# Optimization experiments

Hardware: AMD Instinct MI355X
Metric: run time of the kernel (lower is better)

The kernel has to match this reference:

```python
import jax, jax.numpy as jnp
import numpy as np

NUM_HEADS = 16

def setup_inputs() -> dict:
    key = jax.random.key(0)
    ks = jax.random.split(key, 5)
    B, N, C = 2, 2048, 1024
    x = jax.random.normal(ks[0], (B, N, C), dtype=jnp.float32)
    s_in = 1.0 / np.sqrt(C)
    Wq = jax.random.normal(ks[1], (C, 2 * C), dtype=jnp.float32) * s_in
    Wk = jax.random.normal(ks[2], (C, 2 * C), dtype=jnp.float32) * s_in
    Wv = jax.random.normal(ks[3], (C, 2 * C), dtype=jnp.float32) * s_in
    Wo = jax.random.normal(ks[4], (2 * C, C), dtype=jnp.float32) * (1.0 / np.sqrt(2 * C))
    return {"x": x, "Wq": Wq, "Wk": Wk, "Wv": Wv, "Wo": Wo}

def reference(x, Wq, Wk, Wv, Wo):
    B, N, C = x.shape
    H = NUM_HEADS
    hd = C // H  # head_dim
    def proj(W):
        # [B,N,2C] -> [B,H,N,2*hd]
        return (x @ W).reshape(B, N, H, 2 * hd).transpose(0, 2, 1, 3)
    q = proj(Wq)
    k = proj(Wk)
    v = proj(Wv)
    q_r, q_i = q[..., :hd], q[..., hd:]
    k_r, k_i = k[..., :hd], k[..., hd:]
    v_r, v_i = v[..., :hd], v[..., hd:]
    # complex inner product real part: Re(Q K^H) = q_r.k_r + q_i.k_i
    scores = (jnp.einsum('bhnd,bhmd->bhnm', q_r, k_r)
              + jnp.einsum('bhnd,bhmd->bhnm', q_i, k_i)) / jnp.sqrt(jnp.float32(hd))
    causal = jnp.tril(jnp.ones((N, N), dtype=bool))  # [N,N]
    scores = jnp.where(causal[None, None], scores, -jnp.inf)
    probs = jax.nn.softmax(scores, axis=-1)  # dropout off (eval mode)
    out_r = jnp.einsum('bhnm,bhmd->bhnd', probs, v_r)
    out_i = jnp.einsum('bhnm,bhmd->bhnd', probs, v_i)
    out = jnp.concatenate([out_r, out_i], axis=-1)  # [B,H,N,2*hd]
    out = out.transpose(0, 2, 1, 3).reshape(B, N, 2 * C)
    return out @ Wo  # [B,N,C]
```

## Files before the change

### kernel.cpp

```cpp
#include <hip/hip_runtime.h>
#include <hip/hip_bf16.h>
#include <stdint.h>
#include <cmath>

using bf16 = __hip_bfloat16;
typedef __attribute__((ext_vector_type(8))) short bf16x8;
typedef __attribute__((ext_vector_type(4))) short bf16x4;
typedef __attribute__((ext_vector_type(4))) float f32x4;

#define MFMA16(a, b, c) __builtin_amdgcn_mfma_f32_16x16x32_bf16(a, b, c, 0, 0, 0)

#if defined(__has_builtin)
#if __has_builtin(__builtin_amdgcn_mfma_f32_16x16x16bf16_1k)
#define HAVE_MFMA_K16 1
#endif
#endif
#ifndef HAVE_MFMA_K16
#define HAVE_MFMA_K16 0
#endif

#define NEG_BIG (-1e30f)

__device__ __forceinline__ short f2bf(float v) {
  return __builtin_bit_cast(short, __float2bfloat16(v));
}

__device__ __forceinline__ f32x4 pv_mfma(bf16x4 va, bf16x4 pb, f32x4 c) {
#if HAVE_MFMA_K16
  return __builtin_amdgcn_mfma_f32_16x16x16bf16_1k(va, pb, c, 0, 0, 0);
#else
  const bf16x8 a = {va[0], va[1], va[2], va[3], 0, 0, 0, 0};
  const bf16x8 b = {pb[0], pb[1], pb[2], pb[3], 0, 0, 0, 0};
  return MFMA16(a, b, c);
#endif
}

__device__ __forceinline__ void async_ld16(const bf16* g, bf16* l) {
  __builtin_amdgcn_global_load_lds(
      (const __attribute__((address_space(1))) unsigned int*)g,
      (__attribute__((address_space(3))) unsigned int*)l, 16, 0, 0);
}

template <typename T> __device__ __forceinline__ T cvt_out(float v);
template <> __device__ __forceinline__ float cvt_out<float>(float v) { return v; }
template <> __device__ __forceinline__ bf16 cvt_out<bf16>(float v) { return __float2bfloat16(v); }

__global__ void prep(const float* __restrict__ x,
                     const float* __restrict__ Wq, const float* __restrict__ Wk,
                     const float* __restrict__ Wv, const float* __restrict__ Wo,
                     bf16* __restrict__ xb, bf16* __restrict__ tq,
                     bf16* __restrict__ tk, bf16* __restrict__ tv,
                     bf16* __restrict__ to_) {
  __shared__ bf16 tile[32][33];
  const int bid = blockIdx.x;
  if (bid < 8192) {
    const int z = bid >> 11, tt = bid & 2047;
    const float* in = z == 0 ? Wq : z == 1 ? Wk : z == 2 ? Wv : Wo;
    bf16* out = z == 0 ? tq : z == 1 ? tk : z == 2 ? tv : to_;
    int R, Cc, c0, r0;
    if (z < 3) { R = 1024; Cc = 2048; c0 = (tt & 63) * 32; r0 = (tt >> 6) * 32; }
    else       { R = 2048; Cc = 1024; c0 = (tt & 31) * 32; r0 = (tt >> 5) * 32; }
    const int xx = threadIdx.x & 31;
    const int y = threadIdx.x >> 5;
#pragma unroll
    for (int yy = y; yy < 32; yy += 8)
      tile[yy][xx] = __float2bfloat16(in[(size_t)(r0 + yy) * Cc + c0 + xx]);
    __syncthreads();
#pragma unroll
    for (int yy = y; yy < 32; yy += 8)
      out[(size_t)(c0 + yy) * R + r0 + xx] = tile[xx][yy];
  } else {
    const int i = (bid - 8192) * 256 + threadIdx.x;
    const float4 v = ((const float4*)x)[i];
    bf16 o[4] = {__float2bfloat16(v.x), __float2bfloat16(v.y),
                 __float2bfloat16(v.z), __float2bfloat16(v.w)};
    *(uint64_t*)&xb[i * 4] = *(const uint64_t*)o;
  }
}

__global__ __launch_bounds__(256)
void gemm_qkv(const bf16* __restrict__ xb, const bf16* __restrict__ wq,
              const bf16* __restrict__ wk, const bf16* __restrict__ wv,
              bf16* __restrict__ qo, bf16* __restrict__ ko, bf16* __restrict__ vo) {
  __shared__ __align__(16) bf16 As[128 * 32];
  __shared__ __align__(16) bf16 Bs[128 * 32];
  const int op = blockIdx.y;
  const int bid = blockIdx.x;
  const bf16 *A, *B;
  int m0, n0;
  if (op < 2) { A = xb; B = op ? wk : wq; m0 = (bid >> 4) * 128; n0 = (bid & 15) * 128; }
  else        { A = wv; B = xb;           m0 = (bid & 15) * 128; n0 = (bid >> 4) * 128; }
  const int K = 1024;

  const int t = threadIdx.x;
  const int l = t & 63, w = t >> 6;
  const int q4 = l >> 4, li = l & 15;
  const int wr = (w >> 1) * 64, wc = (w & 1) * 64;

  f32x4 acc[4][4] = {};
  const int colst = (t & 3) * 8;
  const bf16* gA = A + (size_t)m0 * K;
  const bf16* gB = B + (size_t)n0 * K;

  for (int k0 = 0; k0 < K; k0 += 32) {
#pragma unroll
    for (int p = 0; p < 2; ++p) {
      const int row = p * 64 + (t >> 2);
      const int lbase = p * 2048 + (t & ~63) * 8;
      async_ld16(gA + (size_t)row * K + k0 + colst, &As[lbase]);
      async_ld16(gB + (size_t)row * K + k0 + colst, &Bs[lbase]);
    }
    __syncthreads();
    bf16x8 af[4], bfr[4];
#pragma unroll
    for (int i = 0; i < 4; ++i)
      af[i] = *(const bf16x8*)&As[(wr + i * 16 + li) * 32 + q4 * 8];
#pragma unroll
    for (int j = 0; j < 4; ++j)
      bfr[j] = *(const bf16x8*)&Bs[(wc + j * 16 + li) * 32 + q4 * 8];
#pragma unroll
    for (int i = 0; i < 4; ++i)
#pragma unroll
      for (int j = 0; j < 4; ++j)
        acc[i][j] = MFMA16(af[i], bfr[j], acc[i][j]);
    __syncthreads();
  }

#pragma unroll
  for (int i = 0; i < 4; ++i)
#pragma unroll
    for (int j = 0; j < 4; ++j)
#pragma unroll
      for (int r = 0; r < 4; ++r) {
        const int gm = m0 + wr + i * 16 + q4 * 4 + r;
        const int gn = n0 + wc + j * 16 + li;
        const bf16 v = __float2bfloat16(acc[i][j][r]);
        if (op < 2) {
          const int b = gm >> 11, nn = gm & 2047;
          const int h = gn >> 7, d = gn & 127;
          (op ? ko : qo)[((size_t)(b * 16 + h) * 2048 + nn) * 128 + d] = v;
        } else {
          const int h = gm >> 7, d = gm & 127;
          const int b = gn >> 11, nn = gn & 2047;
          vo[((size_t)(b * 16 + h) * 128 + d) * 2048 + nn] = v;
        }
      }
}

template <int NT, typename OT>
__global__ __launch_bounds__(256)
void gemm_bt(const bf16* __restrict__ A, const bf16* __restrict__ B,
             OT* __restrict__ C, int M, int N, int K) {
  __shared__ __align__(16) bf16 As[128 * 32];
  __shared__ __align__(16) bf16 Bs[NT * 32];
  constexpr int JN = NT / 32;
  const int t = threadIdx.x;
  const int l = t & 63, w = t >> 6;
  const int q4 = l >> 4, li = l & 15;
  const int m0 = blockIdx.y * 128;
  const int n0 = blockIdx.x * NT;
  const int wr = (w >> 1) * 64, wc = (w & 1) * (NT / 2);

  f32x4 acc[4][JN] = {};
  const int colst = (t & 3) * 8;
  const bf16* gA = A + (size_t)m0 * K;
  const bf16* gB = B + (size_t)n0 * K;

  for (int k0 = 0; k0 < K; k0 += 32) {
#pragma unroll
    for (int p = 0; p < 2; ++p) {
      const int row = p * 64 + (t >> 2);
      const int lbase = p * 2048 + (t & ~63) * 8;
      async_ld16(gA + (size_t)row * K + k0 + colst, &As[lbase]);
    }
#pragma unroll
    for (int p = 0; p < NT / 64; ++p) {
      const int row = p * 64 + (t >> 2);
      const int lbase = p * 2048 + (t & ~63) * 8;
      async_ld16(gB + (size_t)row * K + k0 + colst, &Bs[lbase]);
    }
    __syncthreads();
    bf16x8 af[4], bfr[JN];
#pragma unroll
    for (int i = 0; i < 4; ++i)
      af[i] = *(const bf16x8*)&As[(wr + i * 16 + li) * 32 + q4 * 8];
#pragma unroll
    for (int j = 0; j < JN; ++j)
      bfr[j] = *(const bf16x8*)&Bs[(wc + j * 16 + li) * 32 + q4 * 8];
#pragma unroll
    for (int i = 0; i < 4; ++i)
#pragma unroll
      for (int j = 0; j < JN; ++j)
        acc[i][j] = MFMA16(af[i], bfr[j], acc[i][j]);
    __syncthreads();
  }

#pragma unroll
  for (int i = 0; i < 4; ++i)
#pragma unroll
    for (int j = 0; j < JN; ++j)
#pragma unroll
      for (int r = 0; r < 4; ++r) {
        const int gm = m0 + wr + i * 16 + q4 * 4 + r;
        const int gn = n0 + wc + j * 16 + li;
        C[(size_t)gm * N + gn] = cvt_out<OT>(acc[i][j][r]);
      }
}

#define VSTR 72

__global__ __launch_bounds__(256, 2)
void flash_attn(const bf16* __restrict__ qm, const bf16* __restrict__ km,
                const bf16* __restrict__ vtm, bf16* __restrict__ om) {
  __shared__ __align__(16) bf16 Ks[64 * 128];
  __shared__ __align__(16) bf16 Vts[128 * VSTR];

  const int t = threadIdx.x;
  const int l = t & 63, w = t >> 6;
  const int q4 = l >> 4, li = l & 15;
  const int bh = blockIdx.x;
  const int y = blockIdx.y;
  const int qt = (y < 8) ? 15 - y : y - 8;
  const int qs = qt * 128;
  const size_t qkbase = (size_t)bh * 2048 * 128;
  const size_t vbase = (size_t)bh * 128 * 2048;
  const int b = bh >> 4, h = bh & 15;

  bf16x8 qf[2][4];
#pragma unroll
  for (int g = 0; g < 2; ++g) {
    const bf16* Qb = qm + qkbase + (size_t)(qs + w * 32 + g * 16 + li) * 128;
#pragma unroll
    for (int f = 0; f < 4; ++f)
      qf[g][f] = *(const bf16x8*)(Qb + f * 32 + q4 * 8);
  }

  f32x4 O[2][8] = {};
  float mrun[2] = {NEG_BIG, NEG_BIG}, lrun[2] = {0.f, 0.f};
  const int gmq[2] = {qs + w * 32 + li, qs + w * 32 + 16 + li};

  const int ktmax = 2 * qt + 1;
  for (int kt = 0; kt <= ktmax; ++kt) {
    const int kn = kt * 64;
#pragma unroll
    for (int p = 0; p < 4; ++p) {
      const int L = p * 256 + t;
      {
        const int row = L >> 4, c = L & 15;
        *(bf16x8*)&Ks[row * 128 + ((c ^ (row & 7)) * 8)] =
            *(const bf16x8*)(km + qkbase + (size_t)(kn + row) * 128 + c * 8);
      }
      {
        const int row = L >> 3, c = L & 7;
        *(bf16x8*)&Vts[row * VSTR + c * 8] =
            *(const bf16x8*)(vtm + vbase + (size_t)row * 2048 + kn + c * 8);
      }
    }
    __syncthreads();

    f32x4 S[2][4];
#pragma unroll
    for (int jk = 0; jk < 4; ++jk) {
      bf16x8 kf[4];
#pragma unroll
      for (int f = 0; f < 4; ++f)
        kf[f] = *(const bf16x8*)&Ks[(jk * 16 + li) * 128 + (((f * 4 + q4) ^ (li & 7)) * 8)];
#pragma unroll
      for (int g = 0; g < 2; ++g) {
        f32x4 s = {0.f, 0.f, 0.f, 0.f};
#pragma unroll
        for (int f = 0; f < 4; ++f) s = MFMA16(kf[f], qf[g][f], s);
        S[g][jk] = s;
      }
    }

    bf16x4 pb[2][4];
#pragma unroll
    for (int g = 0; g < 2; ++g) {
      const bool needmask = (kn + 63) > (qs + w * 32 + g * 16);
      float pv[16];
      float mx = NEG_BIG;
#pragma unroll
      for (int jk = 0; jk < 4; ++jk)
#pragma unroll
        for (int r = 0; r < 4; ++r) {
          float sv = S[g][jk][r] * 0.125f;
          if (needmask && (kn + jk * 16 + q4 * 4 + r) > gmq[g]) sv = NEG_BIG;
          pv[jk * 4 + r] = sv;
          mx = fmaxf(mx, sv);
        }
      mx = fmaxf(mx, __shfl_xor(mx, 16));
      mx = fmaxf(mx, __shfl_xor(mx, 32));
      const float nm = fmaxf(mrun[g], mx);
      const float alpha = __expf(mrun[g] - nm);
      mrun[g] = nm;
      float rs = 0.f;
#pragma unroll
      for (int jk = 0; jk < 4; ++jk)
#pragma unroll
        for (int r = 0; r < 4; ++r) {
          const float e = __expf(pv[jk * 4 + r] - nm);
          rs += e;
          pb[g][jk][r] = f2bf(e);
        }
      rs += __shfl_xor(rs, 16);
      rs += __shfl_xor(rs, 32);
      lrun[g] = lrun[g] * alpha + rs;
#pragma unroll
      for (int dt = 0; dt < 8; ++dt) O[g][dt] *= alpha;
    }

#pragma unroll
    for (int dt = 0; dt < 8; ++dt)
#pragma unroll
      for (int kc = 0; kc < 4; ++kc) {
        const bf16x4 va = *(const bf16x4*)&Vts[(dt * 16 + li) * VSTR + kc * 16 + q4 * 4];
        O[0][dt] = pv_mfma(va, pb[0][kc], O[0][dt]);
        O[1][dt] = pv_mfma(va, pb[1][kc], O[1][dt]);
      }
    __syncthreads();
  }

#pragma unroll
  for (int g = 0; g < 2; ++g) {
    const float inv = 1.0f / lrun[g];
    const size_t orow = (size_t)(b * 2048 + qs + w * 32 + g * 16 + li) * 2048 + h * 128;
#pragma unroll
    for (int dt = 0; dt < 8; ++dt) {
      bf16x4 o4;
#pragma unroll
      for (int r = 0; r < 4; ++r) o4[r] = f2bf(O[g][dt][r] * inv);
      *(bf16x4*)&om[orow + dt * 16 + q4 * 4] = o4;
    }
  }
}

extern "C" void kernel_launch(void* const* d_in, const int* in_sizes, int n_in,
                              void* d_out, int out_size, void* d_ws, size_t ws_size,
                              hipStream_t stream) {
  const float* x = (const float*)d_in[0];
  const float* Wq = (const float*)d_in[1];
  const float* Wk = (const float*)d_in[2];
  const float* Wv = (const float*)d_in[3];
  const float* Wo = (const float*)d_in[4];
  float* out = (float*)d_out;

  bf16* ws = (bf16*)d_ws;
  const size_t MEG = 1u << 20;
  bf16* xb = ws;
  bf16* wTq = ws + 4 * MEG;
  bf16* wTk = ws + 6 * MEG;
  bf16* wTv = ws + 8 * MEG;
  bf16* woT = ws + 10 * MEG;
  bf16* at_ws = ws + 2 * MEG;
  bf16* q_ws = ws + 12 * MEG;
  bf16* k_ws = ws + 20 * MEG;
  bf16* vt_ws = ws + 28 * MEG;

  const dim3 blk(256);

  prep<<<dim3(12288), blk, 0, stream>>>(x, Wq, Wk, Wv, Wo, xb, wTq, wTk, wTv, woT);
  gemm_qkv<<<dim3(512, 3), blk, 0, stream>>>(xb, wTq, wTk, wTv, q_ws, k_ws, vt_ws);
  flash_attn<<<dim3(32, 16), blk, 0, stream>>>(q_ws, k_ws, vt_ws, at_ws);
  gemm_bt<64, float><<<dim3(16, 32), blk, 0, stream>>>(at_ws, woT, out, 4096, 1024, 2048);
}
```

Measured before the change: 276.9 us.

## Use 128-wide KV tiles, exp2 softmax, lazy rescale, and swizzled V layout

Doubles the KV tile from 64 to 128 keys per iteration, which halves the loop trips and barriers. The V^T tile now uses an XOR-swizzled layout in place of the padded stride. Softmax folds the 1/sqrt(d) scale into a single exp2 FMA and masks only on the diagonal tile. The O/l rescale is skipped when no lane's running max moved. In exchange, LDS use grows to 64KB per block and register pressure rises, which may hurt occupancy with two blocks per CU.

```diff
diff --git a/kernel.cpp b/kernel.cpp
--- a/kernel.cpp
+++ b/kernel.cpp
@@ -14,12 +14,19 @@
 #if __has_builtin(__builtin_amdgcn_mfma_f32_16x16x16bf16_1k)
 #define HAVE_MFMA_K16 1
 #endif
+#if __has_builtin(__builtin_amdgcn_exp2f)
+#define EXP2F __builtin_amdgcn_exp2f
+#endif
 #endif
 #ifndef HAVE_MFMA_K16
 #define HAVE_MFMA_K16 0
 #endif
+#ifndef EXP2F
+#define EXP2F exp2f
+#endif
 
 #define NEG_BIG (-1e30f)
+#define K2SCALE 0.18033688011112042f
 
 __device__ __forceinline__ short f2bf(float v) {
   return __builtin_bit_cast(short, __float2bfloat16(v));
@@ -207,13 +214,11 @@
       }
 }
 
-#define VSTR 72
-
 __global__ __launch_bounds__(256, 2)
 void flash_attn(const bf16* __restrict__ qm, const bf16* __restrict__ km,
                 const bf16* __restrict__ vtm, bf16* __restrict__ om) {
-  __shared__ __align__(16) bf16 Ks[64 * 128];
-  __shared__ __align__(16) bf16 Vts[128 * VSTR];
+  __shared__ __align__(16) bf16 Ks[128 * 128];
+  __shared__ __align__(16) bf16 Vts[128 * 128];
 
   const int t = threadIdx.x;
   const int l = t & 63, w = t >> 6;
@@ -239,28 +244,23 @@
   float mrun[2] = {NEG_BIG, NEG_BIG}, lrun[2] = {0.f, 0.f};
   const int gmq[2] = {qs + w * 32 + li, qs + w * 32 + 16 + li};
 
-  const int ktmax = 2 * qt + 1;
-  for (int kt = 0; kt <= ktmax; ++kt) {
-    const int kn = kt * 64;
-#pragma unroll
-    for (int p = 0; p < 4; ++p) {
+  for (int kt = 0; kt <= qt; ++kt) {
+    const int kn = kt * 128;
+#pragma unroll
+    for (int p = 0; p < 8; ++p) {
       const int L = p * 256 + t;
-      {
-        const int row = L >> 4, c = L & 15;
-        *(bf16x8*)&Ks[row * 128 + ((c ^ (row & 7)) * 8)] =
-            *(const bf16x8*)(km + qkbase + (size_t)(kn + row) * 128 + c * 8);
-      }
-      {
-        const int row = L >> 3, c = L & 7;
-        *(bf16x8*)&Vts[row * VSTR + c * 8] =
-            *(const bf16x8*)(vtm + vbase + (size_t)row * 2048 + kn + c * 8);
-      }
-    }
-    __syncthreads();
-
-    f32x4 S[2][4];
-#pragma unroll
-    for (int jk = 0; jk < 4; ++jk) {
+      const int row = L >> 4, c = L & 15;
+      const int j = c ^ (row & 7);
+      *(bf16x8*)&Ks[row * 128 + j * 8] =
+          *(const bf16x8*)(km + qkbase + (size_t)(kn + row) * 128 + c * 8);
+      *(bf16x8*)&Vts[row * 128 + j * 8] =
+          *(const bf16x8*)(vtm + vbase + (size_t)row * 2048 + kn + c * 8);
+    }
+    __syncthreads();
+
+    f32x4 S[2][8];
+#pragma unroll
+    for (int jk = 0; jk < 8; ++jk) {
       bf16x8 kf[4];
 #pragma unroll
       for (int f = 0; f < 4; ++f)
@@ -274,47 +274,67 @@
       }
     }
 
-    bf16x4 pb[2][4];
+    const bool diag = (kt == qt);
+    bf16x4 pb[2][8];
+    float mold[2], nmv[2], rsv[2];
+    bool nomove = true;
 #pragma unroll
     for (int g = 0; g < 2; ++g) {
-      const bool needmask = (kn + 63) > (qs + w * 32 + g * 16);
-      float pv[16];
+      if (diag) {
+#pragma unroll
+        for (int jk = 0; jk < 8; ++jk)
+#pragma unroll
+          for (int r = 0; r < 4; ++r)
+            if ((kn + jk * 16 + q4 * 4 + r) > gmq[g]) S[g][jk][r] = NEG_BIG;
+      }
       float mx = NEG_BIG;
 #pragma unroll
-      for (int jk = 0; jk < 4; ++jk)
-#pragma unroll
-        for (int r = 0; r < 4; ++r) {
-          float sv = S[g][jk][r] * 0.125f;
-          if (needmask && (kn + jk * 16 + q4 * 4 + r) > gmq[g]) sv = NEG_BIG;
-          pv[jk * 4 + r] = sv;
-          mx = fmaxf(mx, sv);
-        }
+      for (int jk = 0; jk < 8; ++jk) {
+        mx = fmaxf(mx, fmaxf(fmaxf(S[g][jk][0], S[g][jk][1]),
+                             fmaxf(S[g][jk][2], S[g][jk][3])));
+      }
       mx = fmaxf(mx, __shfl_xor(mx, 16));
       mx = fmaxf(mx, __shfl_xor(mx, 32));
+      mold[g] = mrun[g];
       const float nm = fmaxf(mrun[g], mx);
-      const float alpha = __expf(mrun[g] - nm);
+      nomove = nomove && (mx <= mold[g]);
       mrun[g] = nm;
+      nmv[g] = nm;
+      const float nmk = nm * K2SCALE;
       float rs = 0.f;
 #pragma unroll
-      for (int jk = 0; jk < 4; ++jk)
+      for (int jk = 0; jk < 8; ++jk)
 #pragma unroll
         for (int r = 0; r < 4; ++r) {
-          const float e = __expf(pv[jk * 4 + r] - nm);
+          const float e = EXP2F(__builtin_fmaf(S[g][jk][r], K2SCALE, -nmk));
           rs += e;
           pb[g][jk][r] = f2bf(e);
         }
       rs += __shfl_xor(rs, 16);
       rs += __shfl_xor(rs, 32);
-      lrun[g] = lrun[g] * alpha + rs;
-#pragma unroll
-      for (int dt = 0; dt < 8; ++dt) O[g][dt] *= alpha;
+      rsv[g] = rs;
+    }
+
+    if (__all(nomove)) {
+      lrun[0] += rsv[0];
+      lrun[1] += rsv[1];
+    } else {
+#pragma unroll
+      for (int g = 0; g < 2; ++g) {
+        const float alpha = EXP2F((mold[g] - nmv[g]) * K2SCALE);
+        lrun[g] = lrun[g] * alpha + rsv[g];
+#pragma unroll
+        for (int dt = 0; dt < 8; ++dt) O[g][dt] *= alpha;
+      }
     }
 
 #pragma unroll
     for (int dt = 0; dt < 8; ++dt)
 #pragma unroll
-      for (int kc = 0; kc < 4; ++kc) {
-        const bf16x4 va = *(const bf16x4*)&Vts[(dt * 16 + li) * VSTR + kc * 16 + q4 * 4];
+      for (int kc = 0; kc < 8; ++kc) {
+        const bf16x4 va = *(const bf16x4*)&Vts[(dt * 16 + li) * 128 +
+                                               (((kc * 2 + (q4 >> 1)) ^ (li & 7)) * 8) +
+                                               (q4 & 1) * 4];
         O[0][dt] = pv_mfma(va, pb[0][kc], O[0][dt]);
         O[1][dt] = pv_mfma(va, pb[1][kc], O[1][dt]);
       }
```

After: 308.5 us. +11.4%, slower.
